# Kernel tuning notes

Hardware: AMD Instinct MI355X
Metric: run time of the kernel (lower is better)

The kernel has to match this reference:

```python
import jax, jax.numpy as jnp
import numpy as np

N_NODES = 100_000
N_EDGES = 3_200_000
D = 64           # node and edge feature dim
HID = 36         # hk.nets.MLP hidden size
OUT = 2          # hk.nets.MLP output size
IN_DIM = 3 * D   # nodes + sent_agg + received_agg (globals are None)


def setup_inputs() -> dict:
    key = jax.random.key(0)
    k_n, k_e, k_s, k_r, k_w1, k_w2 = jax.random.split(key, 6)
    nodes = jax.random.normal(k_n, (N_NODES, D), dtype=jnp.float32)
    edges = jax.random.normal(k_e, (N_EDGES, D), dtype=jnp.float32)
    senders = jax.random.randint(k_s, (N_EDGES,), 0, N_NODES, dtype=jnp.int32)
    receivers = jax.random.randint(k_r, (N_EDGES,), 0, N_NODES, dtype=jnp.int32)
    # haiku Linear default init: truncated normal with stddev 1/sqrt(fan_in); plain normal is fine as a stand-in
    W1 = jax.random.normal(k_w1, (IN_DIM, HID), dtype=jnp.float32) / np.sqrt(IN_DIM)
    b1 = jnp.zeros((HID,), dtype=jnp.float32)
    W2 = jax.random.normal(k_w2, (HID, OUT), dtype=jnp.float32) / np.sqrt(HID)
    b2 = jnp.zeros((OUT,), dtype=jnp.float32)
    return {"nodes": nodes, "edges": edges, "senders": senders,
            "receivers": receivers, "W1": W1, "b1": b1, "W2": W2, "b2": b2}


def reference(nodes, edges, senders, receivers, W1, b1, W2, b2):
    # jraph.GraphNetwork node update with update_edge_fn=None, update_global_fn=None:
    #   sent_attributes     = segment_sum(edges, senders,   num_segments=N)
    #   received_attributes = segment_sum(edges, receivers, num_segments=N)
    #   new_nodes = MLP(concat([nodes, sent, received], axis=-1))
    n = nodes.shape[0]
    sent = jax.ops.segment_sum(edges, senders, num_segments=n)       # [N, D]
    recv = jax.ops.segment_sum(edges, receivers, num_segments=n)     # [N, D]
    feats = jnp.concatenate([nodes, sent, recv], axis=-1)            # [N, 3D]
    h = jax.nn.relu(feats @ W1 + b1)                                 # [N, 36]
    new_nodes = h @ W2 + b2                                          # [N, 2] (activate_final=False)
    return new_nodes
```

## Files before the change

### kernel.cpp

```cpp
#include <hip/hip_runtime.h>
#include <hip/hip_bf16.h>

#define D      64
#define HID    36
#define IN_DIM 192
#define NPB    64
#define MAXNB  2048
#define CHUNK  4096
#define SLICE  64

__global__ void zero_ws_kernel(float4* __restrict__ p, long n4) {
    long i = (long)blockIdx.x * blockDim.x + threadIdx.x;
    long stride = (long)gridDim.x * blockDim.x;
    float4 z = make_float4(0.f, 0.f, 0.f, 0.f);
    for (; i < n4; i += stride) p[i] = z;
}

__global__ __launch_bounds__(256) void scatter_kernel(
    const float* __restrict__ edges,
    const int* __restrict__ senders,
    const int* __restrict__ receivers,
    float* __restrict__ sent,
    float* __restrict__ recv,
    long total)
{
    long i = (long)blockIdx.x * blockDim.x + threadIdx.x;
    if (i >= total) return;
    long e = i >> 6;
    int  d = (int)(i & 63);
    float v = edges[i];
    unsafeAtomicAdd(&sent[(long)senders[e] * D + d], v);
    unsafeAtomicAdd(&recv[(long)receivers[e] * D + d], v);
}

__global__ __launch_bounds__(256) void count_kernel(
    const int* __restrict__ senders,
    const int* __restrict__ receivers,
    int* __restrict__ counts,
    int NB, long E, long total_items)
{
    __shared__ int hist[MAXNB];
    for (int b = threadIdx.x; b < NB; b += 256) hist[b] = 0;
    __syncthreads();

    long start = (long)blockIdx.x * CHUNK;
    long end = start + CHUNK; if (end > total_items) end = total_items;
    for (long i = start + threadIdx.x; i < end; i += 256) {
        int node = (i < E) ? senders[i] : receivers[i - E];
        atomicAdd(&hist[node >> 6], 1);
    }
    __syncthreads();
    int* row = counts + (long)blockIdx.x * NB;
    for (int b = threadIdx.x; b < NB; b += 256) row[b] = hist[b];
}

__global__ __launch_bounds__(256) void colscan1_kernel(
    int* __restrict__ counts, int* __restrict__ psum, int NB, int nblocks)
{
    int b = blockIdx.x * 256 + threadIdx.x;
    if (b >= NB) return;
    int s = blockIdx.y;
    int r0 = s * SLICE;
    int r1 = r0 + SLICE; if (r1 > nblocks) r1 = nblocks;
    int run = 0;
    for (int blk = r0; blk < r1; ++blk) {
        long idx = (long)blk * NB + b;
        int c = counts[idx];
        counts[idx] = run;
        run += c;
    }
    psum[(long)s * NB + b] = run;
}

__global__ __launch_bounds__(256) void colscan2_kernel(
    int* __restrict__ psum, int* __restrict__ tot, int NB, int S)
{
    int b = blockIdx.x * 256 + threadIdx.x;
    if (b >= NB) return;
    int run = 0;
    for (int s = 0; s < S; ++s) {
        long i = (long)s * NB + b;
        int v = psum[i];
        psum[i] = run;
        run += v;
    }
    tot[b] = run;
}

__global__ __launch_bounds__(1024) void basescan_kernel(
    const int* __restrict__ tot, int* __restrict__ base, int NB)
{
    __shared__ int sA[2][MAXNB];
    int t = threadIdx.x;
    sA[0][t]        = (t < NB) ? tot[t] : 0;
    sA[0][t + 1024] = (t + 1024 < NB) ? tot[t + 1024] : 0;
    __syncthreads();
    int src = 0;
    for (int off = 1; off < MAXNB; off <<= 1) {
        int dst = src ^ 1;
        int i0 = t, i1 = t + 1024;
        sA[dst][i0] = sA[src][i0] + ((i0 >= off) ? sA[src][i0 - off] : 0);
        sA[dst][i1] = sA[src][i1] + ((i1 >= off) ? sA[src][i1 - off] : 0);
        src = dst;
        __syncthreads();
    }
    if (t < NB)        base[t]        = (t == 0) ? 0 : sA[src][t - 1];
    if (t + 1024 < NB) base[t + 1024] = sA[src][t + 1023];
}

__global__ __launch_bounds__(256) void scatter_ids_kernel(
    const int* __restrict__ senders,
    const int* __restrict__ receivers,
    const int* __restrict__ counts,
    const int* __restrict__ psum,
    const int* __restrict__ base,
    unsigned* __restrict__ pool,
    int NB, long E, long total_items)
{
    __shared__ int cursor[MAXNB];
    const int* row = counts + (long)blockIdx.x * NB;
    const int* srow = psum + (long)(blockIdx.x / SLICE) * NB;
    for (int b = threadIdx.x; b < NB; b += 256)
        cursor[b] = row[b] + srow[b] + base[b];
    __syncthreads();

    long start = (long)blockIdx.x * CHUNK;
    long end = start + CHUNK; if (end > total_items) end = total_items;
    for (long i = start + threadIdx.x; i < end; i += 256) {
        int dir, node; long edge;
        if (i < E) { dir = 0; edge = i;     node = senders[i]; }
        else       { dir = 1; edge = i - E; node = receivers[i - E]; }
        int b = node >> 6;
        int pos = atomicAdd(&cursor[b], 1);
        pool[pos] = ((unsigned)edge << 7) | ((unsigned)dir << 6) | (unsigned)(node & 63);
    }
}

__global__ __launch_bounds__(256) void sort_bucket_kernel(
    const unsigned* __restrict__ pool,
    const int* __restrict__ base,
    const int* __restrict__ tot,
    unsigned* __restrict__ pool2,
    int4* __restrict__ seg,
    int n_nodes)
{
    __shared__ int hist[4][128];
    __shared__ int cursor[4][128];
    __shared__ int off[128], comb[128], tmp[128];

    int b = blockIdx.x, tid = threadIdx.x;
    int w = tid >> 6, lane = tid & 63;
    int bstart = base[b], cnt = tot[b];

    ((int*)hist)[tid] = 0;
    ((int*)hist)[tid + 256] = 0;
    __syncthreads();

    int q = (cnt + 3) >> 2;
    int rs = w * q;
    int re = rs + q; if (re > cnt) re = cnt;

    for (int i = rs + lane; i < re; i += 64) {
        unsigned r = pool[bstart + i];
        int key = ((r & 63) << 1) | ((r >> 6) & 1);
        atomicAdd(&hist[w][key], 1);
    }
    __syncthreads();

    if (tid < 128) {
        comb[tid] = hist[0][tid] + hist[1][tid] + hist[2][tid] + hist[3][tid];
        tmp[tid] = comb[tid];
    }
    __syncthreads();
    for (int d = 1; d < 128; d <<= 1) {
        int v = 0;
        if (tid < 128) v = (tid >= d) ? tmp[tid - d] : 0;
        __syncthreads();
        if (tid < 128) tmp[tid] += v;
        __syncthreads();
    }
    if (tid < 128) {
        int o = tmp[tid] - comb[tid];
        off[tid] = o;
        int c0 = o + hist[0][tid];
        int c1 = c0 + hist[1][tid];
        int c2 = c1 + hist[2][tid];
        cursor[0][tid] = o;
        cursor[1][tid] = c0;
        cursor[2][tid] = c1;
        cursor[3][tid] = c2;
    }
    __syncthreads();

    if (tid < 64) {
        int node = b * NPB + tid;
        if (node < n_nodes) {
            seg[node] = make_int4(bstart + off[tid * 2],     comb[tid * 2],
                                  bstart + off[tid * 2 + 1], comb[tid * 2 + 1]);
        }
    }

    for (int i = rs + lane; i < re; i += 64) {
        unsigned r = pool[bstart + i];
        int key = ((r & 63) << 1) | ((r >> 6) & 1);
        int pos = atomicAdd(&cursor[w][key], 1);
        pool2[bstart + pos] = r >> 7;
    }
}

__global__ __launch_bounds__(256) void gather_kernel(
    const float* __restrict__ edges,
    const unsigned* __restrict__ pool2,
    const int4* __restrict__ seg,
    float* __restrict__ sent,
    float* __restrict__ recv,
    int n_nodes)
{
    int node = blockIdx.x * 4 + (threadIdx.x >> 6);
    int lane = threadIdx.x & 63;
    if (node >= n_nodes) return;

    int4 si = seg[node];

    float accs = 0.f;
    {
        int s = si.x, c = si.y, j = 0;
        for (; j + 8 <= c; j += 8) {
            unsigned e0 = pool2[s+j],   e1 = pool2[s+j+1], e2 = pool2[s+j+2], e3 = pool2[s+j+3];
            unsigned e4 = pool2[s+j+4], e5 = pool2[s+j+5], e6 = pool2[s+j+6], e7 = pool2[s+j+7];
            float v0 = edges[(long)e0 * D + lane];
            float v1 = edges[(long)e1 * D + lane];
            float v2 = edges[(long)e2 * D + lane];
            float v3 = edges[(long)e3 * D + lane];
            float v4 = edges[(long)e4 * D + lane];
            float v5 = edges[(long)e5 * D + lane];
            float v6 = edges[(long)e6 * D + lane];
            float v7 = edges[(long)e7 * D + lane];
            accs += ((v0 + v1) + (v2 + v3)) + ((v4 + v5) + (v6 + v7));
        }
        for (; j + 4 <= c; j += 4) {
            unsigned e0 = pool2[s+j], e1 = pool2[s+j+1], e2 = pool2[s+j+2], e3 = pool2[s+j+3];
            float v0 = edges[(long)e0 * D + lane];
            float v1 = edges[(long)e1 * D + lane];
            float v2 = edges[(long)e2 * D + lane];
            float v3 = edges[(long)e3 * D + lane];
            accs += (v0 + v1) + (v2 + v3);
        }
        for (; j < c; ++j) accs += edges[(long)pool2[s+j] * D + lane];
    }

    float accr = 0.f;
    {
        int s = si.z, c = si.w, j = 0;
        for (; j + 8 <= c; j += 8) {
            unsigned e0 = pool2[s+j],   e1 = pool2[s+j+1], e2 = pool2[s+j+2], e3 = pool2[s+j+3];
            unsigned e4 = pool2[s+j+4], e5 = pool2[s+j+5], e6 = pool2[s+j+6], e7 = pool2[s+j+7];
            float v0 = edges[(long)e0 * D + lane];
            float v1 = edges[(long)e1 * D + lane];
            float v2 = edges[(long)e2 * D + lane];
            float v3 = edges[(long)e3 * D + lane];
            float v4 = edges[(long)e4 * D + lane];
            float v5 = edges[(long)e5 * D + lane];
            float v6 = edges[(long)e6 * D + lane];
            float v7 = edges[(long)e7 * D + lane];
            accr += ((v0 + v1) + (v2 + v3)) + ((v4 + v5) + (v6 + v7));
        }
        for (; j + 4 <= c; j += 4) {
            unsigned e0 = pool2[s+j], e1 = pool2[s+j+1], e2 = pool2[s+j+2], e3 = pool2[s+j+3];
            float v0 = edges[(long)e0 * D + lane];
            float v1 = edges[(long)e1 * D + lane];
            float v2 = edges[(long)e2 * D + lane];
            float v3 = edges[(long)e3 * D + lane];
            accr += (v0 + v1) + (v2 + v3);
        }
        for (; j < c; ++j) accr += edges[(long)pool2[s+j] * D + lane];
    }

    sent[(long)node * D + lane] = accs;
    recv[(long)node * D + lane] = accr;
}

__global__ __launch_bounds__(256) void mlp_kernel(
    const float* __restrict__ nodes,
    const float* __restrict__ sent,
    const float* __restrict__ recv,
    const float* __restrict__ W1,
    const float* __restrict__ b1,
    const float* __restrict__ W2,
    const float* __restrict__ b2,
    float* __restrict__ out,
    int n)
{
    __shared__ float sW1[IN_DIM * HID];
    __shared__ float sb1[HID];
    __shared__ float sW2[HID * 2];
    __shared__ float sb2[2];

    for (int t = threadIdx.x; t < IN_DIM * HID; t += blockDim.x) sW1[t] = W1[t];
    if (threadIdx.x < HID)     sb1[threadIdx.x] = b1[threadIdx.x];
    if (threadIdx.x < HID * 2) sW2[threadIdx.x] = W2[threadIdx.x];
    if (threadIdx.x < 2)       sb2[threadIdx.x] = b2[threadIdx.x];
    __syncthreads();

    int node = blockIdx.x * blockDim.x + threadIdx.x;
    if (node >= n) return;

    float acc[HID];
#pragma unroll
    for (int j = 0; j < HID; ++j) acc[j] = sb1[j];

#pragma unroll
    for (int part = 0; part < 3; ++part) {
        const float* f = (part == 0 ? nodes : (part == 1 ? sent : recv)) + (long)node * D;
        const float* w = sW1 + part * D * HID;
        for (int k = 0; k < D; k += 4) {
            float4 fv = *reinterpret_cast<const float4*>(f + k);
#pragma unroll
            for (int j = 0; j < HID; ++j) {
                acc[j] += fv.x * w[(k + 0) * HID + j];
                acc[j] += fv.y * w[(k + 1) * HID + j];
                acc[j] += fv.z * w[(k + 2) * HID + j];
                acc[j] += fv.w * w[(k + 3) * HID + j];
            }
        }
    }

    float o0 = sb2[0], o1 = sb2[1];
#pragma unroll
    for (int j = 0; j < HID; ++j) {
        float h = fmaxf(acc[j], 0.f);
        o0 += h * sW2[j * 2 + 0];
        o1 += h * sW2[j * 2 + 1];
    }
    reinterpret_cast<float2*>(out)[node] = make_float2(o0, o1);
}

extern "C" void kernel_launch(void* const* d_in, const int* in_sizes, int n_in,
                              void* d_out, int out_size, void* d_ws, size_t ws_size,
                              hipStream_t stream) {
    const float* nodes     = (const float*)d_in[0];
    const float* edges     = (const float*)d_in[1];
    const int*   senders   = (const int*)d_in[2];
    const int*   receivers = (const int*)d_in[3];
    const float* W1        = (const float*)d_in[4];
    const float* b1        = (const float*)d_in[5];
    const float* W2        = (const float*)d_in[6];
    const float* b2        = (const float*)d_in[7];
    float* out = (float*)d_out;

    const int  n_nodes = in_sizes[0] / D;
    const long E       = in_sizes[2];
    const long total_items = 2 * E;

    const int NB      = (n_nodes + NPB - 1) / NPB;
    const int nblocks = (int)((total_items + CHUNK - 1) / CHUNK);
    const int S       = (nblocks + SLICE - 1) / SLICE;

    const size_t sz_sent = (size_t)n_nodes * D * sizeof(float);
    const size_t sz_pool = (size_t)total_items * sizeof(unsigned);
    const size_t sz_seg  = (size_t)n_nodes * sizeof(int4);
    const size_t sz_nb   = (size_t)MAXNB * sizeof(int);
    const size_t sz_psum = (size_t)S * NB * sizeof(int);
    const size_t need    = 2 * sz_sent + 2 * sz_pool + sz_seg + 2 * sz_nb + sz_psum;
    const size_t sz_counts = (size_t)nblocks * NB * sizeof(int);

    char* wp = (char*)d_ws;
    float*    sent  = (float*)wp;           wp += sz_sent;
    float*    recv  = (float*)wp;           wp += sz_sent;
    unsigned* pool  = (unsigned*)wp;        wp += sz_pool;
    unsigned* pool2 = (unsigned*)wp;        wp += sz_pool;
    int4*     seg   = (int4*)wp;            wp += sz_seg;
    int*      tot   = (int*)wp;             wp += sz_nb;
    int*      base  = (int*)wp;             wp += sz_nb;
    int*      psum  = (int*)wp;
    int*      counts = (int*)sent;

    if (ws_size < need || NB > MAXNB || sz_counts > sz_sent) {
        long n4 = (long)n_nodes * D * 2 / 4;
        zero_ws_kernel<<<2048, 256, 0, stream>>>((float4*)d_ws, n4);
        long total = E * D;
        scatter_kernel<<<(int)((total + 255) / 256), 256, 0, stream>>>(
            edges, senders, receivers, sent, recv, total);
        mlp_kernel<<<(n_nodes + 255) / 256, 256, 0, stream>>>(
            nodes, sent, recv, W1, b1, W2, b2, out, n_nodes);
        return;
    }

    count_kernel<<<nblocks, 256, 0, stream>>>(senders, receivers, counts,
                                              NB, E, total_items);
    {
        dim3 g1((NB + 255) / 256, S);
        colscan1_kernel<<<g1, 256, 0, stream>>>(counts, psum, NB, nblocks);
        colscan2_kernel<<<(NB + 255) / 256, 256, 0, stream>>>(psum, tot, NB, S);
    }
    basescan_kernel<<<1, 1024, 0, stream>>>(tot, base, NB);
    scatter_ids_kernel<<<nblocks, 256, 0, stream>>>(senders, receivers, counts,
                                                    psum, base, pool, NB, E, total_items);
    sort_bucket_kernel<<<NB, 256, 0, stream>>>(pool, base, tot, pool2, seg, n_nodes);
    gather_kernel<<<(n_nodes + 3) / 4, 256, 0, stream>>>(edges, pool2, seg,
                                                         sent, recv, n_nodes);
    mlp_kernel<<<(n_nodes + 255) / 256, 256, 0, stream>>>(
        nodes, sent, recv, W1, b1, W2, b2, out, n_nodes);
}
```

Before: 553.6 us.

## Fuse gather and MLP into one wave-per-node kernel with LDS-staged edge ids

```diff
diff --git a/kernel.cpp b/kernel.cpp
--- a/kernel.cpp
+++ b/kernel.cpp
@@ -208,76 +208,92 @@
     }
 }
 
-__global__ __launch_bounds__(256) void gather_kernel(
+__global__ __launch_bounds__(256) void gmlp_kernel(
     const float* __restrict__ edges,
     const unsigned* __restrict__ pool2,
     const int4* __restrict__ seg,
-    float* __restrict__ sent,
-    float* __restrict__ recv,
+    const float* __restrict__ nodes,
+    const float* __restrict__ W1,
+    const float* __restrict__ b1,
+    const float* __restrict__ W2,
+    const float* __restrict__ b2,
+    float* __restrict__ out,
     int n_nodes)
 {
-    int node = blockIdx.x * 4 + (threadIdx.x >> 6);
-    int lane = threadIdx.x & 63;
+    __shared__ unsigned sids[4][128];
+    __shared__ float sfeat[4][IN_DIM];
+
+    int w = threadIdx.x >> 6, lane = threadIdx.x & 63;
+    int node = blockIdx.x * 4 + w;
     if (node >= n_nodes) return;
 
     int4 si = seg[node];
 
-    float accs = 0.f;
-    {
-        int s = si.x, c = si.y, j = 0;
-        for (; j + 8 <= c; j += 8) {
-            unsigned e0 = pool2[s+j],   e1 = pool2[s+j+1], e2 = pool2[s+j+2], e3 = pool2[s+j+3];
-            unsigned e4 = pool2[s+j+4], e5 = pool2[s+j+5], e6 = pool2[s+j+6], e7 = pool2[s+j+7];
-            float v0 = edges[(long)e0 * D + lane];
-            float v1 = edges[(long)e1 * D + lane];
-            float v2 = edges[(long)e2 * D + lane];
-            float v3 = edges[(long)e3 * D + lane];
-            float v4 = edges[(long)e4 * D + lane];
-            float v5 = edges[(long)e5 * D + lane];
-            float v6 = edges[(long)e6 * D + lane];
-            float v7 = edges[(long)e7 * D + lane];
-            accs += ((v0 + v1) + (v2 + v3)) + ((v4 + v5) + (v6 + v7));
+    float acc2[2];
+#pragma unroll
+    for (int dir = 0; dir < 2; ++dir) {
+        int s = dir ? si.z : si.x;
+        int c = dir ? si.w : si.y;
+        float acc = 0.f;
+        for (int b0 = 0; b0 < c; b0 += 128) {
+            int m = c - b0; if (m > 128) m = 128;
+            if (lane < m)      sids[w][lane]      = pool2[s + b0 + lane];
+            if (64 + lane < m) sids[w][64 + lane] = pool2[s + b0 + 64 + lane];
+            int t = 0;
+            for (; t + 8 <= m; t += 8) {
+                unsigned e0 = sids[w][t],     e1 = sids[w][t + 1];
+                unsigned e2 = sids[w][t + 2], e3 = sids[w][t + 3];
+                unsigned e4 = sids[w][t + 4], e5 = sids[w][t + 5];
+                unsigned e6 = sids[w][t + 6], e7 = sids[w][t + 7];
+                float v0 = edges[(long)e0 * D + lane];
+                float v1 = edges[(long)e1 * D + lane];
+                float v2 = edges[(long)e2 * D + lane];
+                float v3 = edges[(long)e3 * D + lane];
+                float v4 = edges[(long)e4 * D + lane];
+                float v5 = edges[(long)e5 * D + lane];
+                float v6 = edges[(long)e6 * D + lane];
+                float v7 = edges[(long)e7 * D + lane];
+                acc += ((v0 + v1) + (v2 + v3)) + ((v4 + v5) + (v6 + v7));
+            }
+            for (; t + 4 <= m; t += 4) {
+                unsigned e0 = sids[w][t],     e1 = sids[w][t + 1];
+                unsigned e2 = sids[w][t + 2], e3 = sids[w][t + 3];
+                float v0 = edges[(long)e0 * D + lane];
+                float v1 = edges[(long)e1 * D + lane];
+                float v2 = edges[(long)e2 * D + lane];
+                float v3 = edges[(long)e3 * D + lane];
+                acc += (v0 + v1) + (v2 + v3);
+            }
+            for (; t < m; ++t) acc += edges[(long)sids[w][t] * D + lane];
         }
-        for (; j + 4 <= c; j += 4) {
-            unsigned e0 = pool2[s+j], e1 = pool2[s+j+1], e2 = pool2[s+j+2], e3 = pool2[s+j+3];
-            float v0 = edges[(long)e0 * D + lane];
-            float v1 = edges[(long)e1 * D + lane];
-            float v2 = edges[(long)e2 * D + lane];
-            float v3 = edges[(long)e3 * D + lane];
-            accs += (v0 + v1) + (v2 + v3);
+        acc2[dir] = acc;
+    }
+
+    float nf = nodes[(long)node * D + lane];
+    sfeat[w][lane]       = nf;
+    sfeat[w][64 + lane]  = acc2[0];
+    sfeat[w][128 + lane] = acc2[1];
+
+    float h = 0.f;
+    if (lane < HID) {
+        float h0 = 0.f, h1 = 0.f, h2 = 0.f, h3 = 0.f;
+        for (int k = 0; k < IN_DIM; k += 4) {
+            h0 += sfeat[w][k]     * W1[(k)     * HID + lane];
+            h1 += sfeat[w][k + 1] * W1[(k + 1) * HID + lane];
+            h2 += sfeat[w][k + 2] * W1[(k + 2) * HID + lane];
+            h3 += sfeat[w][k + 3] * W1[(k + 3) * HID + lane];
         }
-        for (; j < c; ++j) accs += edges[(long)pool2[s+j] * D + lane];
-    }
-
-    float accr = 0.f;
-    {
-        int s = si.z, c = si.w, j = 0;
-        for (; j + 8 <= c; j += 8) {
-            unsigned e0 = pool2[s+j],   e1 = pool2[s+j+1], e2 = pool2[s+j+2], e3 = pool2[s+j+3];
-            unsigned e4 = pool2[s+j+4], e5 = pool2[s+j+5], e6 = pool2[s+j+6], e7 = pool2[s+j+7];
-            float v0 = edges[(long)e0 * D + lane];
-            float v1 = edges[(long)e1 * D + lane];
-            float v2 = edges[(long)e2 * D + lane];
-            float v3 = edges[(long)e3 * D + lane];
-            float v4 = edges[(long)e4 * D + lane];
-            float v5 = edges[(long)e5 * D + lane];
-            float v6 = edges[(long)e6 * D + lane];
-            float v7 = edges[(long)e7 * D + lane];
-            accr += ((v0 + v1) + (v2 + v3)) + ((v4 + v5) + (v6 + v7));
-        }
-        for (; j + 4 <= c; j += 4) {
-            unsigned e0 = pool2[s+j], e1 = pool2[s+j+1], e2 = pool2[s+j+2], e3 = pool2[s+j+3];
-            float v0 = edges[(long)e0 * D + lane];
-            float v1 = edges[(long)e1 * D + lane];
-            float v2 = edges[(long)e2 * D + lane];
-            float v3 = edges[(long)e3 * D + lane];
-            accr += (v0 + v1) + (v2 + v3);
-        }
-        for (; j < c; ++j) accr += edges[(long)pool2[s+j] * D + lane];
-    }
-
-    sent[(long)node * D + lane] = accs;
-    recv[(long)node * D + lane] = accr;
+        h = fmaxf(b1[lane] + ((h0 + h1) + (h2 + h3)), 0.f);
+    }
+    float p0 = (lane < HID) ? h * W2[lane * 2 + 0] : 0.f;
+    float p1 = (lane < HID) ? h * W2[lane * 2 + 1] : 0.f;
+#pragma unroll
+    for (int off = 32; off; off >>= 1) {
+        p0 += __shfl_down(p0, off, 64);
+        p1 += __shfl_down(p1, off, 64);
+    }
+    if (lane == 0)
+        reinterpret_cast<float2*>(out)[node] = make_float2(p0 + b2[0], p1 + b2[1]);
 }
 
 __global__ __launch_bounds__(256) void mlp_kernel(
@@ -312,15 +328,15 @@
 #pragma unroll
     for (int part = 0; part < 3; ++part) {
         const float* f = (part == 0 ? nodes : (part == 1 ? sent : recv)) + (long)node * D;
-        const float* w = sW1 + part * D * HID;
+        const float* wgt = sW1 + part * D * HID;
         for (int k = 0; k < D; k += 4) {
             float4 fv = *reinterpret_cast<const float4*>(f + k);
 #pragma unroll
             for (int j = 0; j < HID; ++j) {
-                acc[j] += fv.x * w[(k + 0) * HID + j];
-                acc[j] += fv.y * w[(k + 1) * HID + j];
-                acc[j] += fv.z * w[(k + 2) * HID + j];
-                acc[j] += fv.w * w[(k + 3) * HID + j];
+                acc[j] += fv.x * wgt[(k + 0) * HID + j];
+                acc[j] += fv.y * wgt[(k + 1) * HID + j];
+                acc[j] += fv.z * wgt[(k + 2) * HID + j];
+                acc[j] += fv.w * wgt[(k + 3) * HID + j];
             }
         }
     }
@@ -397,8 +413,6 @@
     scatter_ids_kernel<<<nblocks, 256, 0, stream>>>(senders, receivers, counts,
                                                     psum, base, pool, NB, E, total_items);
     sort_bucket_kernel<<<NB, 256, 0, stream>>>(pool, base, tot, pool2, seg, n_nodes);
-    gather_kernel<<<(n_nodes + 3) / 4, 256, 0, stream>>>(edges, pool2, seg,
-                                                         sent, recv, n_nodes);
-    mlp_kernel<<<(n_nodes + 255) / 256, 256, 0, stream>>>(
-        nodes, sent, recv, W1, b1, W2, b2, out, n_nodes);
-}
+    gmlp_kernel<<<(n_nodes + 3) / 4, 256, 0, stream>>>(edges, pool2, seg, nodes,
+                                                       W1, b1, W2, b2, out, n_nodes);
+}
```

Result: no change. 546.6 us (-1.3%).
